# Kernel tuning notes

Measured on AMD Instinct MI355X. Metric: run time of the kernel, lower is better.

The kernel has to match this reference:

```python
import jax, jax.numpy as jnp
import numpy as np

B, N, D = 4, 512, 256  # batch, num_diseases, feature_dim == hidden_dim
H = 256                # hidden_dim
EPS = 1e-5

def _layernorm(x, g, b):
    m = jnp.mean(x, axis=-1, keepdims=True)
    v = jnp.mean((x - m) ** 2, axis=-1, keepdims=True)
    return (x - m) * jax.lax.rsqrt(v + EPS) * g + b

def setup_inputs() -> dict:
    key = jax.random.key(0)
    ks = jax.random.split(key, 16)
    s = 0.02
    return {
        "x": jax.random.normal(ks[0], (B, N, D), jnp.float32),
        "area_matrix": jax.random.uniform(ks[1], (B, N), jnp.float32),
        "co_occurrence": jax.random.uniform(ks[2], (N, N), jnp.float32),
        "Wq": jax.random.normal(ks[3], (H, D), jnp.float32) * s,
        "bq": jnp.zeros((H,), jnp.float32),
        "Wk": jax.random.normal(ks[4], (H, D), jnp.float32) * s,
        "bk": jnp.zeros((H,), jnp.float32),
        "Wv": jax.random.normal(ks[5], (H, D), jnp.float32) * s,
        "bv": jnp.zeros((H,), jnp.float32),
        "We1": jax.random.normal(ks[6], (H, 2), jnp.float32) * 0.5,
        "be1": jnp.zeros((H,), jnp.float32),
        "We2": jax.random.normal(ks[7], (1, H), jnp.float32) * s,
        "be2": jnp.zeros((1,), jnp.float32),
        "Wo": jax.random.normal(ks[8], (H, H), jnp.float32) * s,
        "bo": jnp.zeros((H,), jnp.float32),
        "g_ot": jnp.ones((H,), jnp.float32),
        "b_ot": jnp.zeros((H,), jnp.float32),
        "g1": jnp.ones((H,), jnp.float32),
        "b1": jnp.zeros((H,), jnp.float32),
        "g2": jnp.ones((H,), jnp.float32),
        "b2": jnp.zeros((H,), jnp.float32),
    }

def reference(x, area_matrix, co_occurrence, Wq, bq, Wk, bk, Wv, bv,
              We1, be1, We2, be2, Wo, bo, g_ot, b_ot, g1, b1, g2, b2):
    # projections: (B, N, H)
    q = jnp.einsum('bnd,hd->bnh', x, Wq) + bq
    k = jnp.einsum('bnd,hd->bnh', x, Wk) + bk
    v = jnp.einsum('bnd,hd->bnh', x, Wv) + bv
    attn_scores = jnp.einsum('bih,bjh->bij', q, k) / jnp.sqrt(jnp.float32(H))
    # edge inputs: (B, N, N, 2) = stack(broadcast area along last N, broadcast co-occ along batch)
    area = jnp.broadcast_to(area_matrix[:, :, None], (B, N, N))
    co = jnp.broadcast_to(co_occurrence[None], (B, N, N))
    edge_inputs = jnp.stack([area, co], axis=-1)
    h = jax.nn.relu(jnp.einsum('bije,he->bijh', edge_inputs, We1) + be1)
    edge_weights = jax.nn.sigmoid(jnp.einsum('bijh,oh->bijo', h, We2) + be2)[..., 0]
    attn_probs = jax.nn.softmax(attn_scores * edge_weights, axis=-1)  # dropout = identity (eval)
    out = jnp.einsum('bij,bjh->bih', attn_probs, v)
    out = _layernorm(out, g1, b1)
    out = jax.nn.relu(_layernorm(jnp.einsum('bnh,oh->bno', out, Wo) + bo, g_ot, b_ot))
    out = _layernorm(out + x, g2, b2)
    return out
```

## Files before the change

### kernel.cpp

```cpp
#include <hip/hip_runtime.h>

typedef unsigned short u16;
typedef unsigned int u32;

#define NB 4
#define NN 512
#define ND 256
#define NH 256
#define TI 4

typedef __attribute__((ext_vector_type(8))) short short8;
typedef __attribute__((ext_vector_type(4))) float f32x4;

__device__ __forceinline__ u16 bfq(float f) {
    u32 t; __builtin_memcpy(&t, &f, 4);
    u32 r = (t + 0x7FFFu + ((t >> 16) & 1u)) >> 16;
    return (u16)r;
}

__device__ __forceinline__ float waveReduceSum(float v) {
#pragma unroll
    for (int o = 32; o > 0; o >>= 1) v += __shfl_down(v, o);
    return v;
}

__device__ __forceinline__ void blockReduce8(float4& va, float4& vb, float4* red) {
#pragma unroll
    for (int o = 32; o > 0; o >>= 1) {
        va.x += __shfl_down(va.x, o); va.y += __shfl_down(va.y, o);
        va.z += __shfl_down(va.z, o); va.w += __shfl_down(va.w, o);
        vb.x += __shfl_down(vb.x, o); vb.y += __shfl_down(vb.y, o);
        vb.z += __shfl_down(vb.z, o); vb.w += __shfl_down(vb.w, o);
    }
    int wid = threadIdx.x >> 6;
    __syncthreads();
    if ((threadIdx.x & 63) == 0) { red[2 * wid] = va; red[2 * wid + 1] = vb; }
    __syncthreads();
    float4 ra = red[0], rb = red[1];
#pragma unroll
    for (int w = 1; w < 8; ++w) {
        float4 ua = red[2 * w], ub = red[2 * w + 1];
        ra.x += ua.x; ra.y += ua.y; ra.z += ua.z; ra.w += ua.w;
        rb.x += ub.x; rb.y += ub.y; rb.z += ub.z; rb.w += ub.w;
    }
    va = ra; vb = rb;
}

__global__ __launch_bounds__(256) void prep_kernel(
    const float* __restrict__ x, const float* __restrict__ Wq,
    const float* __restrict__ Wk, const float* __restrict__ Wv,
    const float* __restrict__ Wo,
    u16* __restrict__ xb, u16* __restrict__ wb)
{
    const int idx4 = (blockIdx.x * 256 + threadIdx.x) * 4;
    const float* src;
    u16* dst;
    int off;
    if (idx4 < 524288) { src = x; dst = xb; off = idx4; }
    else {
        int u = idx4 - 524288;
        int which = u >> 16; off = u & 65535;
        src = (which == 0) ? Wq : (which == 1) ? Wk : (which == 2) ? Wv : Wo;
        dst = wb + which * 65536;
    }
    float4 f = *(const float4*)(src + off);
    u32 lo = (u32)bfq(f.x) | ((u32)bfq(f.y) << 16);
    u32 hi = (u32)bfq(f.z) | ((u32)bfq(f.w) << 16);
    *(uint2*)(dst + off) = make_uint2(lo, hi);
}

__global__ __launch_bounds__(256) void qkv_mfma(
    const u16* __restrict__ xb, const u16* __restrict__ wb,
    const float* __restrict__ bq, const float* __restrict__ bk, const float* __restrict__ bv,
    u16* __restrict__ qb, u16* __restrict__ kb, u16* __restrict__ vt)
{
    const int lane = threadIdx.x & 63, wave = threadIdx.x >> 6;
    const int r0 = blockIdx.x * 64 + wave * 16;
    const int out0 = blockIdx.y * 16;
    const int which = blockIdx.y >> 4;
    const float* bia = (which == 0) ? bq : (which == 1) ? bk : bv;

    const int m = lane & 15, koff = (lane >> 4) * 8;
    const u16* Ap = xb + (size_t)(r0 + m) * 256 + koff;
    const u16* Bp = wb + which * 65536 + (size_t)((out0 & 255) + m) * 256 + koff;

    f32x4 acc = {0.f, 0.f, 0.f, 0.f};
#pragma unroll
    for (int ks = 0; ks < 8; ++ks) {
        short8 a  = *(const short8*)(Ap + ks * 32);
        short8 bb = *(const short8*)(Bp + ks * 32);
        acc = __builtin_amdgcn_mfma_f32_16x16x32_bf16(a, bb, acc, 0, 0, 0);
    }

    const int oc = (out0 + m) & 255;
    const float bias = bia[oc];
    const int rbase = r0 + (lane >> 4) * 4;
#pragma unroll
    for (int reg = 0; reg < 4; ++reg) {
        int R = rbase + reg;
        u16 val = bfq(acc[reg] + bias);
        if (which == 0)      qb[(size_t)R * 256 + oc] = val;
        else if (which == 1) kb[(size_t)R * 256 + oc] = val;
        else                 vt[((size_t)(R >> 9) * 256 + oc) * 512 + (R & 511)] = val;
    }
}

__global__ __launch_bounds__(256) void s_gemm(
    const u16* __restrict__ qb, const u16* __restrict__ kb, float* __restrict__ S)
{
    const int lane = threadIdx.x & 63, wave = threadIdx.x >> 6;
    const int job = blockIdx.x * 4 + wave;
    const int b = job >> 10, rem = job & 1023;
    const int i0 = (rem >> 5) * 16, j0 = (rem & 31) * 16;
    const int m = lane & 15, koff = (lane >> 4) * 8;
    const u16* Ap = qb + (size_t)(b * 512 + i0 + m) * 256 + koff;
    const u16* Bp = kb + (size_t)(b * 512 + j0 + m) * 256 + koff;

    f32x4 acc = {0.f, 0.f, 0.f, 0.f};
#pragma unroll
    for (int ks = 0; ks < 8; ++ks) {
        short8 a   = *(const short8*)(Ap + ks * 32);
        short8 bb  = *(const short8*)(Bp + ks * 32);
        acc = __builtin_amdgcn_mfma_f32_16x16x32_bf16(a, bb, acc, 0, 0, 0);
    }
    const int col = j0 + m;
    const int rbase = i0 + (lane >> 4) * 4;
#pragma unroll
    for (int reg = 0; reg < 4; ++reg)
        S[(size_t)(b * 512 + rbase + reg) * 512 + col] = acc[reg];
}

#define PSTR 520
#define YSTR 264
__global__ __launch_bounds__(512) void fused_kernel(
    const float* __restrict__ x, const float* __restrict__ area, const float* __restrict__ co,
    const float* __restrict__ We1, const float* __restrict__ be1,
    const float* __restrict__ We2, const float* __restrict__ be2,
    const u16* __restrict__ wob, const float* __restrict__ bo,
    const float* __restrict__ g_ot, const float* __restrict__ b_ot,
    const float* __restrict__ g1, const float* __restrict__ b1,
    const float* __restrict__ g2, const float* __restrict__ b2,
    const float* __restrict__ S, const u16* __restrict__ vt,
    float* __restrict__ out)
{
    const int tid = threadIdx.x;
    const int b = blockIdx.x >> 7;
    const int i0 = (blockIdx.x & 127) << 2;
    const int lane = tid & 63, w = tid >> 6;

    __shared__ float histS[1024], histB[1024];
    __shared__ float pvbuf[1024];
    __shared__ u16 srow16[16 * PSTR];
    __shared__ u16 y16[16 * YSTR];
    __shared__ float4 red8b[16];
    __shared__ float sBaseS[4], sBaseB[4], redA[8], redB[8];

    const float be2f = be2[0];

    histS[tid] = 0.f; histS[tid + 512] = 0.f;
    histB[tid] = 0.f; histB[tid + 512] = 0.f;
    {
        u32* s32 = (u32*)srow16;
        for (int i = tid; i < 4160; i += 512) s32[i] = 0u;
        u32* y32 = (u32*)y16;
        for (int i = tid; i < 2112; i += 512) y32[i] = 0u;
    }
    __syncthreads();

    {
        const int s = tid >> 7, h0 = tid & 127;
        const float a = area[b * NN + i0 + s];
        float baS = 0.f, baB = 0.f;
#pragma unroll
        for (int k = 0; k < 2; ++k) {
            const int h = h0 + 128 * k;
            const float w10 = We1[2 * h], w11 = We1[2 * h + 1];
            const float w2v = We2[h], be1v = be1[h];
            const float al = fmaf(a, w10, be1v);
            const float sl = w11 * w2v, bb = al * w2v;
            if (w11 == 0.f) {
                if (al > 0.f) baB += bb;
            } else {
                float tt = -al / w11;
                if (w11 > 0.f) {
                    if (tt <= 0.f)      { baS += sl; baB += bb; }
                    else if (tt < 1.f) {
                        int u = (int)(tt * 256.f); u = u > 255 ? 255 : u;
                        atomicAdd(&histS[s * 256 + u], sl);
                        atomicAdd(&histB[s * 256 + u], bb);
                    }
                } else {
                    if (tt >= 1.f)      { baS += sl; baB += bb; }
                    else if (tt > 0.f) {
                        baS += sl; baB += bb;
                        int u = (int)(tt * 256.f); u = u > 255 ? 255 : u;
                        atomicAdd(&histS[s * 256 + u], -sl);
                        atomicAdd(&histB[s * 256 + u], -bb);
                    }
                }
            }
        }
        float rS = waveReduceSum(baS), rB = waveReduceSum(baB);
        if (lane == 0) { redA[w] = rS; redB[w] = rB; }
    }
    __syncthreads();
    if (tid < 4) {
        sBaseS[tid] = redA[2 * tid] + redA[2 * tid + 1];
        sBaseB[tid] = redB[2 * tid] + redB[2 * tid + 1];
    }

    {
        const int s = w & 3;
        float* hp = (w < 4) ? histS : histB;
        float b0 = hp[s * 256 + 4 * lane + 0];
        float b1 = hp[s * 256 + 4 * lane + 1];
        float b2 = hp[s * 256 + 4 * lane + 2];
        float b3 = hp[s * 256 + 4 * lane + 3];
        float p0 = b0, p1 = p0 + b1, p2 = p1 + b2, p3 = p2 + b3;
        float incl = p3;
#pragma unroll
        for (int off = 1; off < 64; off <<= 1) {
            float t = __shfl_up(incl, off);
            if (lane >= off) incl += t;
        }
        float excl = incl - p3;
        hp[s * 256 + 4 * lane + 0] = p0 + excl;
        hp[s * 256 + 4 * lane + 1] = p1 + excl;
        hp[s * 256 + 4 * lane + 2] = p2 + excl;
        hp[s * 256 + 4 * lane + 3] = p3 + excl;
    }
    __syncthreads();

    {
        const float* Sp = S + (size_t)(b * NN + i0) * 512 + tid;
#pragma unroll
        for (int ti = 0; ti < TI; ++ti) {
            float c = co[(size_t)(i0 + ti) * NN + tid];
            int u = (int)(c * 256.f); u = u > 255 ? 255 : u;
            float Sg = sBaseS[ti] + histS[ti * 256 + u];
            float Bg = sBaseB[ti] + histB[ti * 256 + u];
            float e = fmaf(c, Sg, Bg) + be2f;
            float ew = 1.f / (1.f + __expf(-e));
            srow16[ti * PSTR + tid] = bfq(__expf(Sp[(size_t)ti * 512] * 0.0625f * ew));
        }
        __syncthreads();
    }

    {
        const int m = lane & 15, koff = (lane >> 4) * 8;
        const int t0 = 2 * w, t1 = 2 * w + 1;
        const u16* B0p = vt + ((size_t)(b * 256 + t0 * 16 + m)) * 512 + koff;
        const u16* B1p = vt + ((size_t)(b * 256 + t1 * 16 + m)) * 512 + koff;
        const u16* Arow = srow16 + m * PSTR + koff;
        f32x4 acc0 = {0.f, 0.f, 0.f, 0.f}, acc1 = {0.f, 0.f, 0.f, 0.f};
#pragma unroll
        for (int ks = 0; ks < 16; ++ks) {
            short8 a  = *(const short8*)(Arow + ks * 32);
            short8 b0 = *(const short8*)(B0p + ks * 32);
            short8 b1 = *(const short8*)(B1p + ks * 32);
            acc0 = __builtin_amdgcn_mfma_f32_16x16x32_bf16(a, b0, acc0, 0, 0, 0);
            acc1 = __builtin_amdgcn_mfma_f32_16x16x32_bf16(a, b1, acc1, 0, 0, 0);
        }
        __syncthreads();
        if (lane < 16) {
#pragma unroll
            for (int reg = 0; reg < 4; ++reg) {
                pvbuf[reg * 256 + t0 * 16 + lane] = acc0[reg];
                pvbuf[reg * 256 + t1 * 16 + lane] = acc1[reg];
            }
        }
        __syncthreads();
    }

    const int hP = tid & 255, half = tid >> 8;
    float4 sa, sb;
    float accv[TI];
#pragma unroll
    for (int ti = 0; ti < TI; ++ti) {
        accv[ti] = (half == 0) ? pvbuf[ti * 256 + hP] : 0.f;
        ((float*)&sa)[ti] = accv[ti];
        ((float*)&sb)[ti] = accv[ti] * accv[ti];
    }
    blockReduce8(sa, sb, red8b);
    if (half == 0) {
        const float g1v = g1[hP], b1v = b1[hP];
#pragma unroll
        for (int ti = 0; ti < TI; ++ti) {
            float mean = ((const float*)&sa)[ti] * (1.f / 256.f);
            float var = fmaxf(((const float*)&sb)[ti] * (1.f / 256.f) - mean * mean, 0.f);
            y16[ti * YSTR + hP] = bfq((accv[ti] - mean) * rsqrtf(var + 1e-5f) * g1v + b1v);
        }
    }
    __syncthreads();

    {
        const int m = lane & 15, koff = (lane >> 4) * 8;
        const int t0 = 2 * w, t1 = 2 * w + 1;
        const u16* B0p = wob + (size_t)(t0 * 16 + m) * 256 + koff;
        const u16* B1p = wob + (size_t)(t1 * 16 + m) * 256 + koff;
        const u16* Arow = y16 + m * YSTR + koff;
        f32x4 acc0 = {0.f, 0.f, 0.f, 0.f}, acc1 = {0.f, 0.f, 0.f, 0.f};
#pragma unroll
        for (int ks = 0; ks < 8; ++ks) {
            short8 a  = *(const short8*)(Arow + ks * 32);
            short8 b0 = *(const short8*)(B0p + ks * 32);
            short8 b1 = *(const short8*)(B1p + ks * 32);
            acc0 = __builtin_amdgcn_mfma_f32_16x16x32_bf16(a, b0, acc0, 0, 0, 0);
            acc1 = __builtin_amdgcn_mfma_f32_16x16x32_bf16(a, b1, acc1, 0, 0, 0);
        }
        __syncthreads();
        if (lane < 16) {
#pragma unroll
            for (int reg = 0; reg < 4; ++reg) {
                pvbuf[reg * 256 + t0 * 16 + lane] = acc0[reg];
                pvbuf[reg * 256 + t1 * 16 + lane] = acc1[reg];
            }
        }
        __syncthreads();
    }

    float acc2[TI];
    {
        const float bov = (half == 0) ? bo[hP] : 0.f;
#pragma unroll
        for (int ti = 0; ti < TI; ++ti) {
            acc2[ti] = (half == 0) ? pvbuf[ti * 256 + hP] + bov : 0.f;
            ((float*)&sa)[ti] = acc2[ti];
            ((float*)&sb)[ti] = acc2[ti] * acc2[ti];
        }
    }
    blockReduce8(sa, sb, red8b);
    float z[TI];
    const float gotv = (half == 0) ? g_ot[hP] : 0.f;
    const float botv = (half == 0) ? b_ot[hP] : 0.f;
#pragma unroll
    for (int ti = 0; ti < TI; ++ti) {
        float mean = ((const float*)&sa)[ti] * (1.f / 256.f);
        float var = fmaxf(((const float*)&sb)[ti] * (1.f / 256.f) - mean * mean, 0.f);
        z[ti] = fmaxf((acc2[ti] - mean) * rsqrtf(var + 1e-5f) * gotv + botv, 0.f);
    }

    float tt[TI];
#pragma unroll
    for (int ti = 0; ti < TI; ++ti) {
        tt[ti] = (half == 0) ? z[ti] + x[(size_t)(b * NN + i0 + ti) * ND + hP] : 0.f;
        ((float*)&sa)[ti] = tt[ti]; ((float*)&sb)[ti] = tt[ti] * tt[ti];
    }
    blockReduce8(sa, sb, red8b);
    if (half == 0) {
        const float g2v = g2[hP], b2v = b2[hP];
#pragma unroll
        for (int ti = 0; ti < TI; ++ti) {
            float mean = ((const float*)&sa)[ti] * (1.f / 256.f);
            float var = fmaxf(((const float*)&sb)[ti] * (1.f / 256.f) - mean * mean, 0.f);
            float o = (tt[ti] - mean) * rsqrtf(var + 1e-5f) * g2v + b2v;
            out[(size_t)(b * NN + i0 + ti) * NH + hP] = o;
        }
    }
}

extern "C" void kernel_launch(void* const* d_in, const int* in_sizes, int n_in,
                              void* d_out, int out_size, void* d_ws, size_t ws_size,
                              hipStream_t stream) {
    const float* x    = (const float*)d_in[0];
    const float* area = (const float*)d_in[1];
    const float* co   = (const float*)d_in[2];
    const float* Wq   = (const float*)d_in[3];
    const float* bq   = (const float*)d_in[4];
    const float* Wk   = (const float*)d_in[5];
    const float* bk   = (const float*)d_in[6];
    const float* Wv   = (const float*)d_in[7];
    const float* bv   = (const float*)d_in[8];
    const float* We1  = (const float*)d_in[9];
    const float* be1  = (const float*)d_in[10];
    const float* We2  = (const float*)d_in[11];
    const float* be2  = (const float*)d_in[12];
    const float* Wo   = (const float*)d_in[13];
    const float* bo   = (const float*)d_in[14];
    const float* g_ot = (const float*)d_in[15];
    const float* b_ot = (const float*)d_in[16];
    const float* g1   = (const float*)d_in[17];
    const float* b1   = (const float*)d_in[18];
    const float* g2   = (const float*)d_in[19];
    const float* b2   = (const float*)d_in[20];

    u16*  xb  = (u16*)d_ws;
    u16*  wb  = xb + (size_t)2048 * 256;
    u16*  qb  = wb + (size_t)4 * 65536;
    u16*  kb  = qb + (size_t)2048 * 256;
    u16*  vt  = kb + (size_t)2048 * 256;
    float* S  = (float*)(vt + (size_t)2048 * 256);

    prep_kernel<<<768, 256, 0, stream>>>(x, Wq, Wk, Wv, Wo, xb, wb);
    qkv_mfma<<<dim3(32, 48), 256, 0, stream>>>(xb, wb, bq, bk, bv, qb, kb, vt);
    s_gemm<<<1024, 256, 0, stream>>>(qb, kb, S);
    fused_kernel<<<NB * NN / TI, 512, 0, stream>>>(x, area, co, We1, be1, We2, be2,
                                                   wb + 3 * 65536, bo,
                                                   g_ot, b_ot, g1, b1, g2, b2,
                                                   S, vt, (float*)d_out);
}
```

Before: 158.8 us.

## Fuse QK^T score GEMM into the fused attention kernel, dropping the S buffer

Removes the separate s_gemm launch and its fp32 score matrix in global memory. Each fused block now computes its own QK^T tile with MFMA, keeping results in registers, then applies the edge-weight and exp step directly from those registers. This avoids writing and re-reading the full score matrix and saves one kernel launch. In exchange, each block computes a 16-row MFMA tile but uses only 4 of those rows, so the score MFMA work rises about fourfold. Every block also re-reads the whole K matrix for its batch, which relies on cache hits to stay cheap.

```diff
diff --git a/kernel.cpp b/kernel.cpp
--- a/kernel.cpp
+++ b/kernel.cpp
@@ -105,31 +105,6 @@
     }
 }
 
-__global__ __launch_bounds__(256) void s_gemm(
-    const u16* __restrict__ qb, const u16* __restrict__ kb, float* __restrict__ S)
-{
-    const int lane = threadIdx.x & 63, wave = threadIdx.x >> 6;
-    const int job = blockIdx.x * 4 + wave;
-    const int b = job >> 10, rem = job & 1023;
-    const int i0 = (rem >> 5) * 16, j0 = (rem & 31) * 16;
-    const int m = lane & 15, koff = (lane >> 4) * 8;
-    const u16* Ap = qb + (size_t)(b * 512 + i0 + m) * 256 + koff;
-    const u16* Bp = kb + (size_t)(b * 512 + j0 + m) * 256 + koff;
-
-    f32x4 acc = {0.f, 0.f, 0.f, 0.f};
-#pragma unroll
-    for (int ks = 0; ks < 8; ++ks) {
-        short8 a   = *(const short8*)(Ap + ks * 32);
-        short8 bb  = *(const short8*)(Bp + ks * 32);
-        acc = __builtin_amdgcn_mfma_f32_16x16x32_bf16(a, bb, acc, 0, 0, 0);
-    }
-    const int col = j0 + m;
-    const int rbase = i0 + (lane >> 4) * 4;
-#pragma unroll
-    for (int reg = 0; reg < 4; ++reg)
-        S[(size_t)(b * 512 + rbase + reg) * 512 + col] = acc[reg];
-}
-
 #define PSTR 520
 #define YSTR 264
 __global__ __launch_bounds__(512) void fused_kernel(
@@ -140,8 +115,8 @@
     const float* __restrict__ g_ot, const float* __restrict__ b_ot,
     const float* __restrict__ g1, const float* __restrict__ b1,
     const float* __restrict__ g2, const float* __restrict__ b2,
-    const float* __restrict__ S, const u16* __restrict__ vt,
-    float* __restrict__ out)
+    const u16* __restrict__ qb, const u16* __restrict__ kb,
+    const u16* __restrict__ vt, float* __restrict__ out)
 {
     const int tid = threadIdx.x;
     const int b = blockIdx.x >> 7;
@@ -203,6 +178,27 @@
         float rS = waveReduceSum(baS), rB = waveReduceSum(baB);
         if (lane == 0) { redA[w] = rS; redB[w] = rB; }
     }
+
+    f32x4 sacc[4];
+    {
+        const int m = lane & 15, koff = (lane >> 4) * 8;
+        const u16* Ap = qb + (size_t)(b * 512 + i0 + m) * 256 + koff;
+        short8 afr[8];
+#pragma unroll
+        for (int ks = 0; ks < 8; ++ks) afr[ks] = *(const short8*)(Ap + ks * 32);
+#pragma unroll
+        for (int t = 0; t < 4; ++t) {
+            const int j0 = (w * 4 + t) * 16;
+            const u16* Bp = kb + (size_t)(b * 512 + j0 + m) * 256 + koff;
+            f32x4 acc = {0.f, 0.f, 0.f, 0.f};
+#pragma unroll
+            for (int ks = 0; ks < 8; ++ks) {
+                short8 bb = *(const short8*)(Bp + ks * 32);
+                acc = __builtin_amdgcn_mfma_f32_16x16x32_bf16(afr[ks], bb, acc, 0, 0, 0);
+            }
+            sacc[t] = acc;
+        }
+    }
     __syncthreads();
     if (tid < 4) {
         sBaseS[tid] = redA[2 * tid] + redA[2 * tid + 1];
@@ -231,20 +227,23 @@
     }
     __syncthreads();
 
-    {
-        const float* Sp = S + (size_t)(b * NN + i0) * 512 + tid;
-#pragma unroll
-        for (int ti = 0; ti < TI; ++ti) {
-            float c = co[(size_t)(i0 + ti) * NN + tid];
-            int u = (int)(c * 256.f); u = u > 255 ? 255 : u;
-            float Sg = sBaseS[ti] + histS[ti * 256 + u];
-            float Bg = sBaseB[ti] + histB[ti * 256 + u];
-            float e = fmaf(c, Sg, Bg) + be2f;
-            float ew = 1.f / (1.f + __expf(-e));
-            srow16[ti * PSTR + tid] = bfq(__expf(Sp[(size_t)ti * 512] * 0.0625f * ew));
-        }
-        __syncthreads();
-    }
+    if (lane < 16) {
+#pragma unroll
+        for (int t = 0; t < 4; ++t) {
+            const int j = (w * 4 + t) * 16 + lane;
+#pragma unroll
+            for (int reg = 0; reg < 4; ++reg) {
+                float c = co[(size_t)(i0 + reg) * NN + j];
+                int u = (int)(c * 256.f); u = u > 255 ? 255 : u;
+                float Sg = sBaseS[reg] + histS[reg * 256 + u];
+                float Bg = sBaseB[reg] + histB[reg * 256 + u];
+                float e = fmaf(c, Sg, Bg) + be2f;
+                float ew = 1.f / (1.f + __expf(-e));
+                srow16[reg * PSTR + j] = bfq(__expf(sacc[t][reg] * 0.0625f * ew));
+            }
+        }
+    }
+    __syncthreads();
 
     {
         const int m = lane & 15, koff = (lane >> 4) * 8;
@@ -389,13 +388,11 @@
     u16*  qb  = wb + (size_t)4 * 65536;
     u16*  kb  = qb + (size_t)2048 * 256;
     u16*  vt  = kb + (size_t)2048 * 256;
-    float* S  = (float*)(vt + (size_t)2048 * 256);
 
     prep_kernel<<<768, 256, 0, stream>>>(x, Wq, Wk, Wv, Wo, xb, wb);
     qkv_mfma<<<dim3(32, 48), 256, 0, stream>>>(xb, wb, bq, bk, bv, qb, kb, vt);
-    s_gemm<<<1024, 256, 0, stream>>>(qb, kb, S);
     fused_kernel<<<NB * NN / TI, 512, 0, stream>>>(x, area, co, We1, be1, We2, be2,
                                                    wb + 3 * 65536, bo,
                                                    g_ot, b_ot, g1, b1, g2, b2,
-                                                   S, vt, (float*)d_out);
-}
+                                                   qb, kb, vt, (float*)d_out);
+}
```

Measured after the change: 162.0 us. Within noise of the previous version (+2.0%).
